# Performance work log

Hardware: AMD Instinct MI355X
Metric: run time of the kernel (lower is better)

## Reference

```python
import jax, jax.numpy as jnp
import numpy as np

IN_FEATURES = 4096
LORA_R = 128
OUT_DIM = 4096
BSZ = 8
SEQ = 2048
LORA_ALPHA = 256
SCALE = float(LORA_ALPHA) / LORA_R  # 2.0


def setup_inputs() -> dict:
    key = jax.random.key(0)
    k1, k2, k3 = jax.random.split(key, 3)
    x = jax.random.normal(k1, (BSZ, SEQ, IN_FEATURES), dtype=jnp.float32)
    graph_rep = jax.random.normal(k2, (BSZ, LORA_R, OUT_DIM), dtype=jnp.float32)
    # lora_down weight, torch Linear convention: [lora_r, in_features]
    W_down = jax.random.normal(k3, (LORA_R, IN_FEATURES), dtype=jnp.float32) * (1.0 / np.sqrt(IN_FEATURES))
    return {"graph_rep": graph_rep, "x": x, "W_down": W_down}


def reference(graph_rep, x, W_down):
    # lora_down: [B, S, in] @ [in, r] -> [B, S, r]  (dropout p=0 / eval mode)
    down = jnp.einsum('bsi,ri->bsr', x.astype(jnp.float32), W_down)
    # per-sample matmul fused into a single batched contraction:
    # [B, S, r] x [B, r, o] -> [B, S, o], scaled by alpha/r
    out = jnp.einsum('bsr,bro->bso', down, graph_rep) * SCALE
    return out
```

## Files before the change

kernel.cpp:

```cpp
#include <hip/hip_runtime.h>
#include <stdint.h>

#define IN_F   4096
#define R_DIM  128
#define OUT_D  4096
#define BSZ    8
#define SEQ    2048
#define M1     (BSZ * SEQ)
#define SCALE  2.0f
#define KSPLIT 8

typedef __attribute__((ext_vector_type(8))) short short8;
typedef __attribute__((ext_vector_type(4))) float f32x4;

static __device__ __forceinline__ unsigned short bf16_1(float f) {
    union { __bf16 h; unsigned short u; } v; v.h = (__bf16)f; return v.u;
}
static __device__ __forceinline__ uint32_t pack2(float a, float b) {
    union { __bf16 h[2]; uint32_t u; } v;
    v.h[0] = (__bf16)a; v.h[1] = (__bf16)b;
    return v.u;
}
static __device__ __forceinline__ float bf16_to_f32(unsigned short h) {
    union { uint32_t u; float f; } v; v.u = ((uint32_t)h) << 16;
    return v.f;
}
static __device__ __forceinline__ int swz16(int r) { return ((r >> 2) ^ r) & 15; }

static __device__ __forceinline__ void gll16(const void* g, void* l) {
    __builtin_amdgcn_global_load_lds(
        (const __attribute__((address_space(1))) void*)g,
        (__attribute__((address_space(3))) void*)l, 16, 0, 0);
}

__global__ __launch_bounds__(256) void k_prep_w(const float* __restrict__ Wd,
                                                unsigned short* __restrict__ wdbf) {
    const int gid = blockIdx.x * 256 + threadIdx.x;
    const float4 v0 = *(const float4*)(Wd + (size_t)gid * 8);
    const float4 v1 = *(const float4*)(Wd + (size_t)gid * 8 + 4);
    uint4 q;
    q.x = pack2(v0.x, v0.y); q.y = pack2(v0.z, v0.w);
    q.z = pack2(v1.x, v1.y); q.w = pack2(v1.z, v1.w);
    *(uint4*)(wdbf + (size_t)gid * 8) = q;
}

__global__ __launch_bounds__(256) void k_prep_gT(const float* __restrict__ g,
                                                 unsigned short* __restrict__ gT) {
    __shared__ unsigned short L[128][132];
    const int tid = threadIdx.x;
    const int b   = blockIdx.x >> 5;
    const int ot  = blockIdx.x & 31;
    const int o0  = ot * 128;

#pragma unroll
    for (int rep = 0; rep < 16; ++rep) {
        const int k  = (tid >> 5) + rep * 8;
        const int ob = (tid & 31) * 4;
        float4 v = *(const float4*)(g + ((size_t)b * R_DIM + k) * OUT_D + o0 + ob);
        L[ob + 0][k] = bf16_1(v.x);
        L[ob + 1][k] = bf16_1(v.y);
        L[ob + 2][k] = bf16_1(v.z);
        L[ob + 3][k] = bf16_1(v.w);
    }
    __syncthreads();

    const int o  = tid >> 1;
    const int jh = tid & 1;
    unsigned short* dst = gT + ((size_t)(b * OUT_D + o0 + o)) * R_DIM;
#pragma unroll
    for (int jj = 0; jj < 8; ++jj) {
        const int c = jh * 8 + jj;
        const int slot = c ^ swz16(o);
        uint2 q0 = *(const uint2*)&L[o][c * 8];
        uint2 q1 = *(const uint2*)&L[o][c * 8 + 4];
        uint4 q; q.x = q0.x; q.y = q0.y; q.z = q1.x; q.w = q1.y;
        *(uint4*)(dst + slot * 8) = q;
    }
}

template <int KSP>
__global__ __launch_bounds__(512, 6) void k_down_v5(const float* __restrict__ x,
                                                    const unsigned short* __restrict__ wdbf,
                                                    unsigned short* __restrict__ part) {
    constexpr int KCHUNK = IN_F / KSP;
    constexpr int NT     = KCHUNK / 64;

    __shared__ unsigned short As[2][64][72];
    __shared__ unsigned short Bs[2][R_DIM * 64];

    const int tid  = threadIdx.x;
    const int lane = tid & 63;
    const int w    = tid >> 6;
    const int wm   = w >> 2;
    const int wn   = w & 3;
    const int mt   = blockIdx.x & 255;
    const int ks   = blockIdx.x >> 8;
    const int row0 = mt * 64;
    const int kbeg = ks * KCHUNK;

    f32x4 acc[2][2];
#pragma unroll
    for (int m = 0; m < 2; ++m)
#pragma unroll
        for (int n = 0; n < 2; ++n)
#pragma unroll
            for (int j = 0; j < 4; ++j) acc[m][n][j] = 0.0f;

    const int arow = tid >> 3;
    const int acol = (tid & 7) << 3;
    const float* asrc = x + (size_t)(row0 + arow) * IN_F + kbeg + acol;

    const int brow = tid >> 3;
    const int bs_s = tid & 7;
    const int bchunk = bs_s ^ (brow & 7);
    const unsigned short* bsrc0 = wdbf + (size_t)brow * IN_F + kbeg + bchunk * 8;
    const unsigned short* bsrc1 = wdbf + (size_t)(brow + 64) * IN_F + kbeg + bchunk * 8;

    float4 ra0, ra1;

    gll16(bsrc0, &Bs[0][tid * 8]);
    gll16(bsrc1, &Bs[0][(tid + 512) * 8]);
    ra0 = *(const float4*)(asrc);
    ra1 = *(const float4*)(asrc + 4);
    {
        uint4 q;
        q.x = pack2(ra0.x, ra0.y); q.y = pack2(ra0.z, ra0.w);
        q.z = pack2(ra1.x, ra1.y); q.w = pack2(ra1.z, ra1.w);
        *(uint4*)&As[0][arow][acol] = q;
    }
    __syncthreads();

    for (int t = 0; t < NT; ++t) {
        const int cur = t & 1, nxt = cur ^ 1;
        if (t + 1 < NT) {
            gll16(bsrc0 + (t + 1) * 64, &Bs[nxt][tid * 8]);
            gll16(bsrc1 + (t + 1) * 64, &Bs[nxt][(tid + 512) * 8]);
            ra0 = *(const float4*)(asrc + (t + 1) * 64);
            ra1 = *(const float4*)(asrc + (t + 1) * 64 + 4);
        }
#pragma unroll
        for (int kk = 0; kk < 64; kk += 32) {
            const int g = lane >> 4;
            const int c = (kk >> 3) + g;
            short8 af[2], bfv[2];
#pragma unroll
            for (int m = 0; m < 2; ++m) {
                const int r = wm * 32 + m * 16 + (lane & 15);
                af[m] = *(const short8*)&As[cur][r][kk + g * 8];
            }
#pragma unroll
            for (int n = 0; n < 2; ++n) {
                const int rB = wn * 32 + n * 16 + (lane & 15);
                const int slot = c ^ (rB & 7);
                bfv[n] = *(const short8*)&Bs[cur][rB * 64 + slot * 8];
            }
#pragma unroll
            for (int m = 0; m < 2; ++m)
#pragma unroll
                for (int n = 0; n < 2; ++n)
                    acc[m][n] = __builtin_amdgcn_mfma_f32_16x16x32_bf16(af[m], bfv[n], acc[m][n], 0, 0, 0);
        }
        if (t + 1 < NT) {
            uint4 q;
            q.x = pack2(ra0.x, ra0.y); q.y = pack2(ra0.z, ra0.w);
            q.z = pack2(ra1.x, ra1.y); q.w = pack2(ra1.z, ra1.w);
            *(uint4*)&As[nxt][arow][acol] = q;
        }
        __syncthreads();
    }

    unsigned short* dst = part + (size_t)ks * M1 * R_DIM;
#pragma unroll
    for (int m = 0; m < 2; ++m)
#pragma unroll
        for (int n = 0; n < 2; ++n)
#pragma unroll
            for (int j = 0; j < 4; ++j) {
                int r = row0 + wm * 32 + m * 16 + ((lane >> 4) << 2) + j;
                int c = wn * 32 + n * 16 + (lane & 15);
                dst[(size_t)r * R_DIM + c] = bf16_1(acc[m][n][j]);
            }
}

template <int KS>
__global__ __launch_bounds__(512) void k_reduce(const unsigned short* __restrict__ part,
                                                unsigned short* __restrict__ down) {
    const size_t chunk = (size_t)blockIdx.x * 512 + threadIdx.x;
    const size_t off = chunk * 8;
    if (off >= (size_t)M1 * R_DIM) return;
    float lo[4] = {0, 0, 0, 0}, hi[4] = {0, 0, 0, 0};
#pragma unroll
    for (int p = 0; p < KS; ++p) {
        uint4 q = *(const uint4*)(part + (size_t)p * M1 * R_DIM + off);
        const uint32_t* a = (const uint32_t*)&q;
#pragma unroll
        for (int i = 0; i < 4; ++i) {
            lo[i] += bf16_to_f32((unsigned short)(a[i] & 0xFFFF));
            hi[i] += bf16_to_f32((unsigned short)(a[i] >> 16));
        }
    }
    uint4 r;
    uint32_t* o = (uint32_t*)&r;
#pragma unroll
    for (int i = 0; i < 4; ++i) o[i] = pack2(lo[i], hi[i]);
    *(uint4*)(down + off) = r;
}

#define BM1 64
#define BK1 64
#define PAD 8
static __device__ __forceinline__ void st_bf16x4(unsigned short* p, float4 v) {
    uint2 q; q.x = pack2(v.x, v.y); q.y = pack2(v.z, v.w);
    *(uint2*)p = q;
}

__global__ __launch_bounds__(512) void k_down(const float* __restrict__ x,
                                              const float* __restrict__ Wd,
                                              unsigned short* __restrict__ down) {
    __shared__ unsigned short As[BM1][BK1 + PAD];
    __shared__ unsigned short Bsh[R_DIM][BK1 + PAD];

    const int tid  = threadIdx.x;
    const int lane = tid & 63;
    const int w    = tid >> 6;
    const int wm   = w >> 2;
    const int wn   = w & 3;
    const int row0 = blockIdx.x * BM1;

    f32x4 acc[2][2];
#pragma unroll
    for (int m = 0; m < 2; ++m)
#pragma unroll
        for (int n = 0; n < 2; ++n)
#pragma unroll
            for (int j = 0; j < 4; ++j) acc[m][n][j] = 0.0f;

    const int arow = tid >> 4;
    const int acol = (tid & 15) << 2;
    float4 ra[2], rb[4];

    ra[0] = *(const float4*)(x + (size_t)(row0 + arow) * IN_F + acol);
    ra[1] = *(const float4*)(x + (size_t)(row0 + arow + 32) * IN_F + acol);
#pragma unroll
    for (int i = 0; i < 4; ++i)
        rb[i] = *(const float4*)(Wd + (size_t)(arow + 32 * i) * IN_F + acol);
    st_bf16x4(&As[arow][acol], ra[0]);
    st_bf16x4(&As[arow + 32][acol], ra[1]);
#pragma unroll
    for (int i = 0; i < 4; ++i) st_bf16x4(&Bsh[arow + 32 * i][acol], rb[i]);
    __syncthreads();

    for (int k0 = BK1; k0 <= IN_F; k0 += BK1) {
        const bool more = (k0 < IN_F);
        if (more) {
            ra[0] = *(const float4*)(x + (size_t)(row0 + arow) * IN_F + k0 + acol);
            ra[1] = *(const float4*)(x + (size_t)(row0 + arow + 32) * IN_F + k0 + acol);
#pragma unroll
            for (int i = 0; i < 4; ++i)
                rb[i] = *(const float4*)(Wd + (size_t)(arow + 32 * i) * IN_F + k0 + acol);
        }
#pragma unroll
        for (int kk = 0; kk < BK1; kk += 32) {
            short8 af[2], bfv[2];
#pragma unroll
            for (int m = 0; m < 2; ++m)
                af[m] = *(const short8*)&As[wm * 32 + m * 16 + (lane & 15)][kk + (lane >> 4) * 8];
#pragma unroll
            for (int n = 0; n < 2; ++n)
                bfv[n] = *(const short8*)&Bsh[wn * 32 + n * 16 + (lane & 15)][kk + (lane >> 4) * 8];
#pragma unroll
            for (int m = 0; m < 2; ++m)
#pragma unroll
                for (int n = 0; n < 2; ++n)
                    acc[m][n] = __builtin_amdgcn_mfma_f32_16x16x32_bf16(af[m], bfv[n], acc[m][n], 0, 0, 0);
        }
        __syncthreads();
        if (more) {
            st_bf16x4(&As[arow][acol], ra[0]);
            st_bf16x4(&As[arow + 32][acol], ra[1]);
#pragma unroll
            for (int i = 0; i < 4; ++i) st_bf16x4(&Bsh[arow + 32 * i][acol], rb[i]);
            __syncthreads();
        }
    }

#pragma unroll
    for (int m = 0; m < 2; ++m)
#pragma unroll
        for (int n = 0; n < 2; ++n)
#pragma unroll
            for (int j = 0; j < 4; ++j) {
                int r = row0 + wm * 32 + m * 16 + ((lane >> 4) << 2) + j;
                int c = wn * 32 + n * 16 + (lane & 15);
                down[(size_t)r * R_DIM + c] = bf16_1(acc[m][n][j]);
            }
}

#define BM2 64
#define BN2 128

__global__ __launch_bounds__(512) void k_out4(const unsigned short* __restrict__ down,
                                              const unsigned short* __restrict__ gT,
                                              float* __restrict__ out) {
    __shared__ __align__(16) unsigned char lraw[49152];
    unsigned short* As  = (unsigned short*)lraw;
    unsigned short* Bsv = (unsigned short*)(lraw + 16384);
    float* Eb = (float*)lraw;

    const int tid  = threadIdx.x;
    const int lane = tid & 63;
    const int w    = tid >> 6;
    const int wm   = w >> 2;
    const int wn   = w & 3;
    const int blk  = blockIdx.x;
    const int o_t  = blk & 31;
    const int s_t  = (blk >> 5) & 31;
    const int b    = blk >> 10;
    const int s0   = s_t * BM2;
    const int o0   = o_t * BN2;

    const unsigned short* bim = gT + ((size_t)(b * OUT_D + o0)) * R_DIM;
#pragma unroll
    for (int r = 0; r < 4; ++r)
        gll16(bim + (r * 512 + tid) * 8, Bsv + (r * 512 + tid) * 8);

    {
        const int rr = tid >> 4;
        const int j  = tid & 15;
        const int sl0 = j ^ swz16(rr);
        const int sl1 = j ^ swz16(rr + 32);
        *(uint4*)&As[rr * R_DIM + sl0 * 8] =
            *(const uint4*)(down + ((size_t)(b * SEQ + s0 + rr) * R_DIM) + j * 8);
        *(uint4*)&As[(rr + 32) * R_DIM + sl1 * 8] =
            *(const uint4*)(down + ((size_t)(b * SEQ + s0 + rr + 32) * R_DIM) + j * 8);
    }
    __syncthreads();

    f32x4 acc[2][2];
#pragma unroll
    for (int m = 0; m < 2; ++m)
#pragma unroll
        for (int n = 0; n < 2; ++n)
#pragma unroll
            for (int j = 0; j < 4; ++j) acc[m][n][j] = 0.0f;

    const int cl = lane & 15;
    const int gq = lane >> 4;
#pragma unroll
    for (int kk = 0; kk < R_DIM; kk += 32) {
        const int cbase = (kk >> 3) + gq;
        short8 af[2], bfv[2];
#pragma unroll
        for (int m = 0; m < 2; ++m) {
            const int r = wm * 32 + m * 16 + cl;
            af[m] = *(const short8*)&As[r * R_DIM + (cbase ^ swz16(r)) * 8];
        }
#pragma unroll
        for (int n = 0; n < 2; ++n) {
            const int o = wn * 32 + n * 16 + cl;
            bfv[n] = *(const short8*)&Bsv[o * R_DIM + (cbase ^ swz16(o)) * 8];
        }
#pragma unroll
        for (int m = 0; m < 2; ++m)
#pragma unroll
            for (int n = 0; n < 2; ++n)
                acc[m][n] = __builtin_amdgcn_mfma_f32_16x16x32_bf16(af[m], bfv[n], acc[m][n], 0, 0, 0);
    }

    __syncthreads();
#pragma unroll
    for (int m = 0; m < 2; ++m)
#pragma unroll
        for (int n = 0; n < 2; ++n)
#pragma unroll
            for (int j = 0; j < 4; ++j) {
                const int s_l = wm * 32 + m * 16 + gq * 4 + j;
                const int o_l = wn * 32 + n * 16 + cl;
                Eb[s_l * 132 + o_l] = SCALE * acc[m][n][j];
            }
    __syncthreads();

    const int l31 = lane & 31;
    const int hi  = lane >> 5;
#pragma unroll
    for (int p = 0; p < 4; ++p) {
        const int row = w * 8 + p * 2 + hi;
        const f32x4 v = *(const f32x4*)&Eb[row * 132 + l31 * 4];
        f32x4* dst = (f32x4*)(out + ((size_t)(b * SEQ + s0 + row)) * OUT_D + o0 + l31 * 4);
        __builtin_nontemporal_store(v, dst);
    }
}

__global__ __launch_bounds__(512) void k_out3(const unsigned short* __restrict__ down,
                                              const float* __restrict__ g,
                                              float* __restrict__ out) {
    __shared__ __align__(16) unsigned char lraw[49152];
    unsigned short* As  = (unsigned short*)lraw;
    unsigned short* Bsv = (unsigned short*)(lraw + 16384);
    float* Eb = (float*)lraw;

    const int tid  = threadIdx.x;
    const int lane = tid & 63;
    const int w    = tid >> 6;
    const int wm   = w >> 2;
    const int wn   = w & 3;
    const int blk  = blockIdx.x;
    const int o_t  = blk & 31;
    const int s_t  = (blk >> 5) & 31;
    const int b    = blk >> 10;
    const int s0   = s_t * BM2;
    const int o0   = o_t * BN2;

    {
        const int rr = tid >> 4;
        const int j  = tid & 15;
        const int sl0 = j ^ swz16(rr);
        const int sl1 = j ^ swz16(rr + 32);
        *(uint4*)&As[rr * R_DIM + sl0 * 8] =
            *(const uint4*)(down + ((size_t)(b * SEQ + s0 + rr) * R_DIM) + j * 8);
        *(uint4*)&As[(rr + 32) * R_DIM + sl1 * 8] =
            *(const uint4*)(down + ((size_t)(b * SEQ + s0 + rr + 32) * R_DIM) + j * 8);
    }
    {
        const int oq  = tid & 31;
        const int kq0 = tid >> 5;
#pragma unroll
        for (int rep = 0; rep < 2; ++rep) {
            const int kq = kq0 + 16 * rep;
            float4 v0 = *(const float4*)(g + ((size_t)b * R_DIM + 4 * kq + 0) * OUT_D + o0 + 4 * oq);
            float4 v1 = *(const float4*)(g + ((size_t)b * R_DIM + 4 * kq + 1) * OUT_D + o0 + 4 * oq);
            float4 v2 = *(const float4*)(g + ((size_t)b * R_DIM + 4 * kq + 2) * OUT_D + o0 + 4 * oq);
            float4 v3 = *(const float4*)(g + ((size_t)b * R_DIM + 4 * kq + 3) * OUT_D + o0 + 4 * oq);
            const float* p0 = (const float*)&v0;
            const float* p1 = (const float*)&v1;
            const float* p2 = (const float*)&v2;
            const float* p3 = (const float*)&v3;
#pragma unroll
            for (int i = 0; i < 4; ++i) {
                const int o = 4 * oq + i;
                uint2 q;
                q.x = pack2(p0[i], p1[i]);
                q.y = pack2(p2[i], p3[i]);
                const int slot = (kq >> 1) ^ swz16(o);
                *(uint2*)&Bsv[o * R_DIM + slot * 8 + (kq & 1) * 4] = q;
            }
        }
    }
    __syncthreads();

    f32x4 acc[2][2];
#pragma unroll
    for (int m = 0; m < 2; ++m)
#pragma unroll
        for (int n = 0; n < 2; ++n)
#pragma unroll
            for (int j = 0; j < 4; ++j) acc[m][n][j] = 0.0f;

    const int cl = lane & 15;
    const int gq = lane >> 4;
#pragma unroll
    for (int kk = 0; kk < R_DIM; kk += 32) {
        const int cbase = (kk >> 3) + gq;
        short8 af[2], bfv[2];
#pragma unroll
        for (int m = 0; m < 2; ++m) {
            const int r = wm * 32 + m * 16 + cl;
            af[m] = *(const short8*)&As[r * R_DIM + (cbase ^ swz16(r)) * 8];
        }
#pragma unroll
        for (int n = 0; n < 2; ++n) {
            const int o = wn * 32 + n * 16 + cl;
            bfv[n] = *(const short8*)&Bsv[o * R_DIM + (cbase ^ swz16(o)) * 8];
        }
#pragma unroll
        for (int m = 0; m < 2; ++m)
#pragma unroll
            for (int n = 0; n < 2; ++n)
                acc[m][n] = __builtin_amdgcn_mfma_f32_16x16x32_bf16(af[m], bfv[n], acc[m][n], 0, 0, 0);
    }

    __syncthreads();
#pragma unroll
    for (int m = 0; m < 2; ++m)
#pragma unroll
        for (int n = 0; n < 2; ++n)
#pragma unroll
            for (int j = 0; j < 4; ++j) {
                const int s_l = wm * 32 + m * 16 + gq * 4 + j;
                const int o_l = wn * 32 + n * 16 + cl;
                Eb[s_l * 132 + o_l] = SCALE * acc[m][n][j];
            }
    __syncthreads();

    const int l31 = lane & 31;
    const int hi  = lane >> 5;
#pragma unroll
    for (int p = 0; p < 4; ++p) {
        const int row = w * 8 + p * 2 + hi;
        const f32x4 v = *(const f32x4*)&Eb[row * 132 + l31 * 4];
        f32x4* dst = (f32x4*)(out + ((size_t)(b * SEQ + s0 + row)) * OUT_D + o0 + l31 * 4);
        __builtin_nontemporal_store(v, dst);
    }
}

extern "C" void kernel_launch(void* const* d_in, const int* in_sizes, int n_in,
                              void* d_out, int out_size, void* d_ws, size_t ws_size,
                              hipStream_t stream) {
    const float* graph_rep = (const float*)d_in[0];
    const float* x         = (const float*)d_in[1];
    const float* Wd        = (const float*)d_in[2];
    float* out             = (float*)d_out;

    const size_t de = (size_t)M1 * R_DIM;
    const size_t we = (size_t)R_DIM * IN_F;
    const size_t ge = (size_t)BSZ * OUT_D * R_DIM;
    const size_t need_full = (9 * de + we + ge) * sizeof(unsigned short);
    const size_t need_mid  = (9 * de + we) * sizeof(unsigned short);
    const int out_grid = BSZ * (SEQ / BM2) * (OUT_D / BN2);

    if (ws_size >= need_full) {
        unsigned short* part = (unsigned short*)d_ws;
        unsigned short* down = part + 8 * de;
        unsigned short* wdbf = part + 9 * de;
        unsigned short* gT   = wdbf + we;
        k_prep_w<<<256, 256, 0, stream>>>(Wd, wdbf);
        k_prep_gT<<<BSZ * 32, 256, 0, stream>>>(graph_rep, gT);
        k_down_v5<8><<<256 * 8, 512, 0, stream>>>(x, wdbf, part);
        k_reduce<8><<<(int)(de / 8 / 512), 512, 0, stream>>>(part, down);
        k_out4<<<out_grid, 512, 0, stream>>>(down, gT, out);
    } else if (ws_size >= need_mid) {
        unsigned short* part = (unsigned short*)d_ws;
        unsigned short* down = part + 8 * de;
        unsigned short* wdbf = part + 9 * de;
        k_prep_w<<<256, 256, 0, stream>>>(Wd, wdbf);
        k_down_v5<8><<<256 * 8, 512, 0, stream>>>(x, wdbf, part);
        k_reduce<8><<<(int)(de / 8 / 512), 512, 0, stream>>>(part, down);
        k_out3<<<out_grid, 512, 0, stream>>>(down, graph_rep, out);
    } else {
        unsigned short* down = (unsigned short*)d_ws;
        k_down<<<M1 / BM1, 512, 0, stream>>>(x, Wd, down);
        k_out3<<<out_grid, 512, 0, stream>>>(down, graph_rep, out);
    }
}
```

Measured before the change: 140.1 us.

## Merge prep kernels, stage split-K epilogue through LDS, pre-swizzle down for async loads

Result: faster. 136.4 us (-2.7%).

```diff
diff --git a/kernel.cpp b/kernel.cpp
--- a/kernel.cpp
+++ b/kernel.cpp
@@ -33,23 +33,25 @@
         (__attribute__((address_space(3))) void*)l, 16, 0, 0);
 }
 
-__global__ __launch_bounds__(256) void k_prep_w(const float* __restrict__ Wd,
-                                                unsigned short* __restrict__ wdbf) {
-    const int gid = blockIdx.x * 256 + threadIdx.x;
-    const float4 v0 = *(const float4*)(Wd + (size_t)gid * 8);
-    const float4 v1 = *(const float4*)(Wd + (size_t)gid * 8 + 4);
-    uint4 q;
-    q.x = pack2(v0.x, v0.y); q.y = pack2(v0.z, v0.w);
-    q.z = pack2(v1.x, v1.y); q.w = pack2(v1.z, v1.w);
-    *(uint4*)(wdbf + (size_t)gid * 8) = q;
-}
-
-__global__ __launch_bounds__(256) void k_prep_gT(const float* __restrict__ g,
-                                                 unsigned short* __restrict__ gT) {
+__global__ __launch_bounds__(256) void k_prep(const float* __restrict__ Wd,
+                                              unsigned short* __restrict__ wdbf,
+                                              const float* __restrict__ g,
+                                              unsigned short* __restrict__ gT) {
     __shared__ unsigned short L[128][132];
     const int tid = threadIdx.x;
-    const int b   = blockIdx.x >> 5;
-    const int ot  = blockIdx.x & 31;
+    if (blockIdx.x < 256) {
+        const int gid = blockIdx.x * 256 + tid;
+        const float4 v0 = *(const float4*)(Wd + (size_t)gid * 8);
+        const float4 v1 = *(const float4*)(Wd + (size_t)gid * 8 + 4);
+        uint4 q;
+        q.x = pack2(v0.x, v0.y); q.y = pack2(v0.z, v0.w);
+        q.z = pack2(v1.x, v1.y); q.w = pack2(v1.z, v1.w);
+        *(uint4*)(wdbf + (size_t)gid * 8) = q;
+        return;
+    }
+    const int bb  = blockIdx.x - 256;
+    const int b   = bb >> 5;
+    const int ot  = bb & 31;
     const int o0  = ot * 128;
 
 #pragma unroll
@@ -169,20 +171,36 @@
         __syncthreads();
     }
 
-    unsigned short* dst = part + (size_t)ks * M1 * R_DIM;
-#pragma unroll
-    for (int m = 0; m < 2; ++m)
-#pragma unroll
-        for (int n = 0; n < 2; ++n)
-#pragma unroll
-            for (int j = 0; j < 4; ++j) {
-                int r = row0 + wm * 32 + m * 16 + ((lane >> 4) << 2) + j;
-                int c = wn * 32 + n * 16 + (lane & 15);
-                dst[(size_t)r * R_DIM + c] = bf16_1(acc[m][n][j]);
-            }
-}
-
-template <int KS>
+    {
+        unsigned short* Eb = &Bs[0][0];
+        const int gq = lane >> 4;
+        const int cl = lane & 15;
+#pragma unroll
+        for (int m = 0; m < 2; ++m)
+#pragma unroll
+            for (int n = 0; n < 2; ++n)
+#pragma unroll
+                for (int j = 0; j < 4; ++j) {
+                    const int r = wm * 32 + m * 16 + gq * 4 + j;
+                    const int c = wn * 32 + n * 16 + cl;
+                    Eb[r * 136 + c] = bf16_1(acc[m][n][j]);
+                }
+    }
+    __syncthreads();
+    {
+        const unsigned short* Eb = &Bs[0][0];
+        const int row = tid >> 3;
+        const int seg = tid & 7;
+        unsigned short* dst = part + (size_t)ks * M1 * R_DIM +
+                              (size_t)(row0 + row) * R_DIM + seg * 16;
+        const uint4 q0 = *(const uint4*)&Eb[row * 136 + seg * 16];
+        const uint4 q1 = *(const uint4*)&Eb[row * 136 + seg * 16 + 8];
+        *(uint4*)(dst)     = q0;
+        *(uint4*)(dst + 8) = q1;
+    }
+}
+
+template <int KS, bool SWZ>
 __global__ __launch_bounds__(512) void k_reduce(const unsigned short* __restrict__ part,
                                                 unsigned short* __restrict__ down) {
     const size_t chunk = (size_t)blockIdx.x * 512 + threadIdx.x;
@@ -203,7 +221,14 @@
     uint32_t* o = (uint32_t*)&r;
 #pragma unroll
     for (int i = 0; i < 4; ++i) o[i] = pack2(lo[i], hi[i]);
-    *(uint4*)(down + off) = r;
+    if (SWZ) {
+        const int row = (int)(off >> 7);
+        const int j   = (int)((off >> 3) & 15);
+        const int slot = j ^ swz16(row & 63);
+        *(uint4*)(down + ((size_t)row << 7) + slot * 8) = r;
+    } else {
+        *(uint4*)(down + off) = r;
+    }
 }
 
 #define BM1 64
@@ -299,7 +324,7 @@
 #define BM2 64
 #define BN2 128
 
-__global__ __launch_bounds__(512) void k_out4(const unsigned short* __restrict__ down,
+__global__ __launch_bounds__(512) void k_out5(const unsigned short* __restrict__ downswz,
                                               const unsigned short* __restrict__ gT,
                                               float* __restrict__ out) {
     __shared__ __align__(16) unsigned char lraw[49152];
@@ -323,17 +348,9 @@
 #pragma unroll
     for (int r = 0; r < 4; ++r)
         gll16(bim + (r * 512 + tid) * 8, Bsv + (r * 512 + tid) * 8);
-
-    {
-        const int rr = tid >> 4;
-        const int j  = tid & 15;
-        const int sl0 = j ^ swz16(rr);
-        const int sl1 = j ^ swz16(rr + 32);
-        *(uint4*)&As[rr * R_DIM + sl0 * 8] =
-            *(const uint4*)(down + ((size_t)(b * SEQ + s0 + rr) * R_DIM) + j * 8);
-        *(uint4*)&As[(rr + 32) * R_DIM + sl1 * 8] =
-            *(const uint4*)(down + ((size_t)(b * SEQ + s0 + rr + 32) * R_DIM) + j * 8);
-    }
+    const unsigned short* aim = downswz + ((size_t)(b * SEQ + s0)) * R_DIM;
+    gll16(aim + tid * 8, As + tid * 8);
+    gll16(aim + (tid + 512) * 8, As + (tid + 512) * 8);
     __syncthreads();
 
     f32x4 acc[2][2];
@@ -523,18 +540,17 @@
         unsigned short* down = part + 8 * de;
         unsigned short* wdbf = part + 9 * de;
         unsigned short* gT   = wdbf + we;
-        k_prep_w<<<256, 256, 0, stream>>>(Wd, wdbf);
-        k_prep_gT<<<BSZ * 32, 256, 0, stream>>>(graph_rep, gT);
+        k_prep<<<256 + BSZ * 32, 256, 0, stream>>>(Wd, wdbf, graph_rep, gT);
         k_down_v5<8><<<256 * 8, 512, 0, stream>>>(x, wdbf, part);
-        k_reduce<8><<<(int)(de / 8 / 512), 512, 0, stream>>>(part, down);
-        k_out4<<<out_grid, 512, 0, stream>>>(down, gT, out);
+        k_reduce<8, true><<<(int)(de / 8 / 512), 512, 0, stream>>>(part, down);
+        k_out5<<<out_grid, 512, 0, stream>>>(down, gT, out);
     } else if (ws_size >= need_mid) {
         unsigned short* part = (unsigned short*)d_ws;
         unsigned short* down = part + 8 * de;
         unsigned short* wdbf = part + 9 * de;
-        k_prep_w<<<256, 256, 0, stream>>>(Wd, wdbf);
+        k_prep<<<256, 256, 0, stream>>>(Wd, wdbf, graph_rep, wdbf);
         k_down_v5<8><<<256 * 8, 512, 0, stream>>>(x, wdbf, part);
-        k_reduce<8><<<(int)(de / 8 / 512), 512, 0, stream>>>(part, down);
+        k_reduce<8, false><<<(int)(de / 8 / 512), 512, 0, stream>>>(part, down);
         k_out3<<<out_grid, 512, 0, stream>>>(down, graph_rep, out);
     } else {
         unsigned short* down = (unsigned short*)d_ws;
```
